# Kernel tuning notes

Measured on AMD Instinct MI355X. Metric: run time of the kernel, lower is better.

Reference implementation:

```python
import jax, jax.numpy as jnp
import numpy as np

EMB = 1024
HEADS = 16
HEAD_DIM = EMB // HEADS
SEQ = 2048
BATCH = 2
EPS = 1e-5


def gelu_tanh(x):
    # 0.5*x*(1+tanh(sqrt(2/pi)*(x+0.044715*x^3)))
    c = jnp.sqrt(jnp.asarray(2.0 / jnp.pi, x.dtype))
    return 0.5 * x * (1.0 + jnp.tanh(c * (x + 0.044715 * x * x * x)))


def layernorm(x, scale, shift):
    mean = jnp.mean(x, axis=-1, keepdims=True)
    # torch var(unbiased=True) -> ddof=1
    var = jnp.var(x, axis=-1, keepdims=True, ddof=1)
    return scale * (x - mean) / jnp.sqrt(var + EPS) + shift


def setup_inputs() -> dict:
    key = jax.random.key(0)
    ks = jax.random.split(key, 12)
    s = 0.02
    d = {
        "x": jax.random.normal(ks[0], (BATCH, SEQ, EMB), jnp.float32),
        "Wq": jax.random.normal(ks[1], (EMB, EMB), jnp.float32) * s,
        "bq": jnp.zeros((EMB,), jnp.float32),
        "Wk": jax.random.normal(ks[2], (EMB, EMB), jnp.float32) * s,
        "bk": jnp.zeros((EMB,), jnp.float32),
        "Wv": jax.random.normal(ks[3], (EMB, EMB), jnp.float32) * s,
        "bv": jnp.zeros((EMB,), jnp.float32),
        "Wo": jax.random.normal(ks[4], (EMB, EMB), jnp.float32) * s,
        "bo": jnp.zeros((EMB,), jnp.float32),
        "W1": jax.random.normal(ks[5], (EMB, 4 * EMB), jnp.float32) * s,
        "b1": jnp.zeros((4 * EMB,), jnp.float32),
        "W2": jax.random.normal(ks[6], (4 * EMB, EMB), jnp.float32) * s,
        "b2": jnp.zeros((EMB,), jnp.float32),
        "ln1_scale": jnp.ones((EMB,), jnp.float32),
        "ln1_shift": jnp.zeros((EMB,), jnp.float32),
        "ln2_scale": jnp.ones((EMB,), jnp.float32),
        "ln2_shift": jnp.zeros((EMB,), jnp.float32),
    }
    return d


def reference(x, Wq, bq, Wk, bk, Wv, bv, Wo, bo, W1, b1, W2, b2,
              ln1_scale, ln1_shift, ln2_scale, ln2_shift):
    b, n, _ = x.shape

    # --- attention sub-block (pre-norm) ---
    h = layernorm(x, ln1_scale, ln1_shift)
    q = (h @ Wq + bq).reshape(b, n, HEADS, HEAD_DIM).transpose(0, 2, 1, 3)
    k = (h @ Wk + bk).reshape(b, n, HEADS, HEAD_DIM).transpose(0, 2, 1, 3)
    v = (h @ Wv + bv).reshape(b, n, HEADS, HEAD_DIM).transpose(0, 2, 1, 3)

    # explicit O(n^2) scores, as in the source
    scores = jnp.einsum("bhqd,bhkd->bhqk", q, k)
    causal = jnp.triu(jnp.ones((n, n), bool), k=1)  # True above diagonal -> masked
    scores = jnp.where(causal, -jnp.inf, scores)
    weights = jax.nn.softmax(scores / jnp.sqrt(jnp.asarray(HEAD_DIM, x.dtype)), axis=-1)
    ctx = jnp.einsum("bhqk,bhkd->bhqd", weights, v)
    ctx = ctx.transpose(0, 2, 1, 3).reshape(b, n, EMB)
    x = x + (ctx @ Wo + bo)  # dropout is identity (rate 0 / eval)

    # --- FFN sub-block (pre-norm) ---
    h = layernorm(x, ln2_scale, ln2_shift)
    h = gelu_tanh(h @ W1 + b1)
    x = x + (h @ W2 + b2)
    return x
```

## Files before the change

kernel.cpp:

```cpp
#include <hip/hip_runtime.h>
#include <hip/hip_bf16.h>

#define EMB 1024
#define SEQ 2048
#define BATCH 2
#define HEADS 16
#define HDIM 64
#define ROWS (BATCH*SEQ)

typedef __hip_bfloat16 bf16;
typedef __bf16 bf16x8 __attribute__((ext_vector_type(8)));
typedef float f32x4 __attribute__((ext_vector_type(4)));

#define AS1 __attribute__((address_space(1)))
#define AS3 __attribute__((address_space(3)))

__device__ __forceinline__ void load_lds16(const void* g, void* l) {
    __builtin_amdgcn_global_load_lds((const AS1 void*)g, (AS3 void*)l, 16, 0, 0);
}

__device__ __forceinline__ float gelu_f(float x) {
    float y = 1.5957691216057308f * (x + 0.044715f * x * x * x);
    return x / (1.0f + __expf(-y));
}

__global__ void transpose_cast_kernel(const float* __restrict__ in, bf16* __restrict__ out,
                                      int R, int C) {
    __shared__ bf16 tile[32][33];
    int tx = threadIdx.x, ty = threadIdx.y;
    int c0 = blockIdx.x * 32, r0 = blockIdx.y * 32;
    for (int i = ty; i < 32; i += 8)
        tile[i][tx] = (bf16)in[(size_t)(r0 + i) * C + c0 + tx];
    __syncthreads();
    for (int i = ty; i < 32; i += 8)
        out[(size_t)(c0 + i) * R + r0 + tx] = tile[tx][i];
}

__global__ void transpose_cast4_kernel(const float* __restrict__ w0, const float* __restrict__ w1,
                                       const float* __restrict__ w2, const float* __restrict__ w3,
                                       bf16* __restrict__ o0, bf16* __restrict__ o1,
                                       bf16* __restrict__ o2, bf16* __restrict__ o3) {
    __shared__ bf16 tile[32][33];
    int z = blockIdx.z;
    const float* in = (z == 0) ? w0 : (z == 1) ? w1 : (z == 2) ? w2 : w3;
    bf16* out = (z == 0) ? o0 : (z == 1) ? o1 : (z == 2) ? o2 : o3;
    int tx = threadIdx.x, ty = threadIdx.y;
    int c0 = blockIdx.x * 32, r0 = blockIdx.y * 32;
    for (int i = ty; i < 32; i += 8)
        tile[i][tx] = (bf16)in[(size_t)(r0 + i) * 1024 + c0 + tx];
    __syncthreads();
    for (int i = ty; i < 32; i += 8)
        out[(size_t)(c0 + i) * 1024 + r0 + tx] = tile[tx][i];
}

__global__ void transpose_v_kernel(const bf16* __restrict__ v, bf16* __restrict__ vt) {
    __shared__ bf16 tile[32][33];
    int tx = threadIdx.x, ty = threadIdx.y;
    int bh = blockIdx.z;
    const bf16* in = v + (size_t)(bh >> 4) * SEQ * EMB + (bh & 15) * HDIM;
    bf16* out = vt + (size_t)bh * HDIM * SEQ;
    int s0 = blockIdx.x * 32, d0 = blockIdx.y * 32;
    for (int i = ty; i < 32; i += 8)
        tile[i][tx] = in[(size_t)(s0 + i) * EMB + d0 + tx];
    __syncthreads();
    for (int i = ty; i < 32; i += 8)
        out[(size_t)(d0 + i) * SEQ + s0 + tx] = tile[tx][i];
}

__global__ __launch_bounds__(256) void layernorm_kernel(const float* __restrict__ x,
                                                        bf16* __restrict__ out,
                                                        const float* __restrict__ scale,
                                                        const float* __restrict__ shift) {
    int row = blockIdx.x;
    int t = threadIdx.x;
    const float* xr = x + (size_t)row * EMB;
    float v[4];
    float s = 0.f, s2 = 0.f;
#pragma unroll
    for (int i = 0; i < 4; i++) {
        v[i] = xr[t + 256 * i];
        s += v[i];
        s2 += v[i] * v[i];
    }
#pragma unroll
    for (int off = 32; off > 0; off >>= 1) {
        s += __shfl_down(s, off);
        s2 += __shfl_down(s2, off);
    }
    __shared__ float sh[8];
    __shared__ float stats[2];
    int lane = t & 63, wid = t >> 6;
    if (lane == 0) { sh[wid] = s; sh[wid + 4] = s2; }
    __syncthreads();
    if (t == 0) {
        float ts = sh[0] + sh[1] + sh[2] + sh[3];
        float ts2 = sh[4] + sh[5] + sh[6] + sh[7];
        float mean = ts / (float)EMB;
        float var = (ts2 - (float)EMB * mean * mean) / (float)(EMB - 1);
        stats[0] = mean;
        stats[1] = rsqrtf(var + 1e-5f);
    }
    __syncthreads();
    float mean = stats[0], inv = stats[1];
#pragma unroll
    for (int i = 0; i < 4; i++) {
        int c = t + 256 * i;
        float y = (v[i] - mean) * inv * scale[c] + shift[c];
        out[(size_t)row * EMB + c] = (bf16)y;
    }
}

__device__ __forceinline__ void swz64(int id, int& bx, int& by) {
    int xcd = id & 7, m = id >> 3;
    by = xcd + 8 * (m & 3) + 32 * (m >> 6);
    bx = (m >> 2) & 15;
}

__device__ __forceinline__ void stage_half(const bf16* g, bf16* lds, int tid, size_t rowK64) {
    load_lds16(g, lds + tid * 8);
    load_lds16(g + rowK64, lds + 4096 + tid * 8);
}

template <int ACT, int QKV>
__global__ __launch_bounds__(512, 2) void gemm256_kernel(
    const bf16* __restrict__ A, const bf16* __restrict__ BT,
    bf16* __restrict__ C0, bf16* __restrict__ C1, bf16* __restrict__ C2,
    const float* __restrict__ bias0, const float* __restrict__ bias1,
    const float* __restrict__ bias2, int N, int K) {
    __shared__ __align__(16) bf16 lA[4][128 * 64];
    __shared__ __align__(16) bf16 lB[4][128 * 64];
    const int tid = threadIdx.x;
    const int wave = tid >> 6, lane = tid & 63;
    const int an = lane & 15, aq = lane >> 4;
    const int wr = wave >> 2, wc = wave & 3;

    int id = blockIdx.x;
    int xcd = id & 7, m = id >> 3;
    int by = xcd * 2 + (m & 1);
    int bx = m >> 1;
    int m0 = by * 256, n0 = bx * 256;

    const int srow = tid >> 3;
    const int csw = ((tid & 7) ^ (srow & 7)) * 8;
    const bf16* Ag = A + (size_t)(m0 + srow) * K + csw;
    const bf16* Bg = BT + (size_t)(n0 + srow) * K + csw;
    const size_t rowK64 = (size_t)64 * K;
    const size_t rowK128 = (size_t)128 * K;

    stage_half(Bg, lB[0], tid, rowK64);
    stage_half(Bg + rowK128, lB[1], tid, rowK64);
    stage_half(Ag, lA[0], tid, rowK64);
    stage_half(Ag + rowK128, lA[1], tid, rowK64);
    stage_half(Bg + 64, lB[2], tid, rowK64);
    stage_half(Bg + rowK128 + 64, lB[3], tid, rowK64);
    asm volatile("s_waitcnt vmcnt(4)" ::: "memory");
    __builtin_amdgcn_s_barrier();

    f32x4 acc[8][4] = {};
    const int NT = K >> 6;
    const int lrB = (wc & 1) * 64;

    for (int t = 0; t < NT; ++t) {
        const bf16* As = lA[(2 * t + wr) & 3];
        const bf16* Bs = lB[(2 * t + (wc >> 1)) & 3];
        bf16x8 bfv[4][2];
#pragma unroll
        for (int p = 0; p < 4; ++p) {
            bf16x8 af[2][2];
            if (p == 0) {
#pragma unroll
                for (int j = 0; j < 4; ++j)
#pragma unroll
                    for (int kk = 0; kk < 2; ++kk) {
                        int r = lrB + 16 * j + an;
                        bfv[j][kk] = *(const bf16x8*)(Bs + r * 64 + ((kk * 4 + aq) ^ (r & 7)) * 8);
                    }
            }
#pragma unroll
            for (int ii = 0; ii < 2; ++ii)
#pragma unroll
                for (int kk = 0; kk < 2; ++kk) {
                    int r = 16 * (2 * p + ii) + an;
                    af[ii][kk] = *(const bf16x8*)(As + r * 64 + ((kk * 4 + aq) ^ (r & 7)) * 8);
                }
            if (p == 0) {
                if (t + 1 < NT)
                    stage_half(Ag + (size_t)(t + 1) * 64, lA[(2 * t + 2) & 3], tid, rowK64);
            } else if (p == 1) {
                if (t + 1 < NT)
                    stage_half(Ag + rowK128 + (size_t)(t + 1) * 64, lA[(2 * t + 3) & 3], tid, rowK64);
            } else if (p == 2) {
                if (t + 2 < NT)
                    stage_half(Bg + (size_t)(t + 2) * 64, lB[(2 * t + 4) & 3], tid, rowK64);
            } else {
                if (t + 2 < NT) {
                    stage_half(Bg + rowK128 + (size_t)(t + 2) * 64, lB[(2 * t + 5) & 3], tid, rowK64);
                    asm volatile("s_waitcnt vmcnt(4)" ::: "memory");
                } else {
                    asm volatile("s_waitcnt vmcnt(0)" ::: "memory");
                }
            }
            __builtin_amdgcn_s_barrier();
            asm volatile("s_waitcnt lgkmcnt(0)" ::: "memory");
            __builtin_amdgcn_s_setprio(1);
#pragma unroll
            for (int ii = 0; ii < 2; ++ii)
#pragma unroll
                for (int j = 0; j < 4; ++j)
#pragma unroll
                    for (int kk = 0; kk < 2; ++kk)
                        acc[2 * p + ii][j] = __builtin_amdgcn_mfma_f32_16x16x32_bf16(
                            af[ii][kk], bfv[j][kk], acc[2 * p + ii][j], 0, 0, 0);
            __builtin_amdgcn_s_setprio(0);
            __builtin_amdgcn_s_barrier();
        }
    }

#pragma unroll
    for (int j = 0; j < 4; ++j) {
        int col = n0 + wc * 64 + 16 * j + an;
        if (QKV == 0) {
            float bv = bias0[col];
#pragma unroll
            for (int i = 0; i < 8; ++i) {
#pragma unroll
                for (int r = 0; r < 4; ++r) {
                    int row = m0 + wr * 128 + 16 * i + aq * 4 + r;
                    float v = acc[i][j][r] + bv;
                    if (ACT == 1) v = gelu_f(v);
                    C0[(size_t)row * N + col] = (bf16)v;
                }
            }
        } else {
            int region = col >> 10, c = col & 1023;
            const float* bp = (region == 0) ? bias0 : (region == 1) ? bias1 : bias2;
            bf16* outp = (region == 0) ? C0 : (region == 1) ? C1 : C2;
            float scl = (region == 0) ? 0.125f : 1.0f;
            float bv = bp[c];
#pragma unroll
            for (int i = 0; i < 8; ++i) {
#pragma unroll
                for (int r = 0; r < 4; ++r) {
                    int row = m0 + wr * 128 + 16 * i + aq * 4 + r;
                    float v = (acc[i][j][r] + bv) * scl;
                    outp[(size_t)row * EMB + c] = (bf16)v;
                }
            }
        }
    }
}

template <int RES, int OUTF>
__global__ __launch_bounds__(256) void gemm64_kernel(const bf16* __restrict__ A,
                                                     const bf16* __restrict__ BT,
                                                     void* __restrict__ Cout,
                                                     const float* __restrict__ bias,
                                                     const float* __restrict__ res,
                                                     int M, int N, int K) {
    __shared__ __align__(16) bf16 lA[2][2][64 * 32];
    __shared__ __align__(16) bf16 lB[2][2][64 * 32];
    int tid = threadIdx.x;
    int wave = tid >> 6, lane = tid & 63;
    int bx, by;
    swz64(blockIdx.x, bx, by);
    int m0 = by * 64, n0 = bx * 64;
    int wm = (wave >> 1) * 32, wn = (wave & 1) * 32;
    f32x4 acc[2][2] = {};

    int srow = wave * 16 + (lane >> 2);
    int skc = (lane & 3) * 8;
    const bf16* Ag = A + (size_t)(m0 + srow) * K + skc;
    const bf16* Bg = BT + (size_t)(n0 + srow) * K + skc;
    size_t woff = (size_t)(wave * 16) * 32;

    const int an = lane & 15;
    const int ak = (lane >> 4) * 8;

    load_lds16(Ag, &lA[0][0][woff]);
    load_lds16(Ag + 32, &lA[0][1][woff]);
    load_lds16(Bg, &lB[0][0][woff]);
    load_lds16(Bg + 32, &lB[0][1][woff]);

    int nsteps = K >> 6;
    for (int t = 0; t < nsteps; t++) {
        int buf = t & 1;
        asm volatile("s_waitcnt vmcnt(0)" ::: "memory");
        __syncthreads();
        if (t + 1 < nsteps) {
            int k0 = (t + 1) * 64;
            load_lds16(Ag + k0, &lA[buf ^ 1][0][woff]);
            load_lds16(Ag + k0 + 32, &lA[buf ^ 1][1][woff]);
            load_lds16(Bg + k0, &lB[buf ^ 1][0][woff]);
            load_lds16(Bg + k0 + 32, &lB[buf ^ 1][1][woff]);
        }
#pragma unroll
        for (int h = 0; h < 2; h++) {
            bf16x8 af[2], bfv[2];
#pragma unroll
            for (int i = 0; i < 2; i++)
                af[i] = *(const bf16x8*)(&lA[buf][h][(wm + 16 * i + an) * 32 + ak]);
#pragma unroll
            for (int j = 0; j < 2; j++)
                bfv[j] = *(const bf16x8*)(&lB[buf][h][(wn + 16 * j + an) * 32 + ak]);
#pragma unroll
            for (int i = 0; i < 2; i++)
#pragma unroll
                for (int j = 0; j < 2; j++)
                    acc[i][j] = __builtin_amdgcn_mfma_f32_16x16x32_bf16(af[i], bfv[j], acc[i][j], 0, 0, 0);
        }
    }
#pragma unroll
    for (int j = 0; j < 2; j++) {
        int col = n0 + wn + 16 * j + an;
        float bv = bias[col];
#pragma unroll
        for (int i = 0; i < 2; i++) {
#pragma unroll
            for (int r = 0; r < 4; r++) {
                int row = m0 + wm + 16 * i + (lane >> 4) * 4 + r;
                float vx = acc[i][j][r] + bv;
                size_t idx = (size_t)row * N + col;
                if (RES == 2) vx += res[idx];
                if (OUTF == 0) ((bf16*)Cout)[idx] = (bf16)vx;
                else ((float*)Cout)[idx] = vx;
            }
        }
    }
}

__global__ __launch_bounds__(256, 4) void attn_kernel(const bf16* __restrict__ q,
                                                      const bf16* __restrict__ k,
                                                      const bf16* __restrict__ vt,
                                                      bf16* __restrict__ ctx) {
    __shared__ __align__(16) bf16 ksm[2][64 * 64];
    __shared__ __align__(16) bf16 vsm[2][64 * 64];
    __shared__ __align__(16) bf16 pbuf[4][16][40];
    int tid = threadIdx.x;
    int wave = tid >> 6, lane = tid & 63;
    int id = blockIdx.x;
    int bh = id >> 5;
    int bx = ((id & 31) + bh) & 31;
    int b = bh >> 4, h = bh & 15;
    int q0 = bx * 64 + wave * 16;
    const bf16* qp = q + (size_t)b * SEQ * EMB + h * HDIM;
    const bf16* kp = k + (size_t)b * SEQ * EMB + h * HDIM;
    const bf16* vp = vt + (size_t)bh * HDIM * SEQ;

    int an = lane & 15, aq = lane >> 4;

    bf16x8 qf0 = *(const bf16x8*)(qp + (size_t)(q0 + an) * EMB + aq * 8);
    bf16x8 qf1 = *(const bf16x8*)(qp + (size_t)(q0 + an) * EMB + 32 + aq * 8);
    f32x4 o[4] = {};
    float lp[4] = {0.f, 0.f, 0.f, 0.f};

    int srow0 = tid >> 3;
    int srow1 = srow0 + 32;
    int sc = tid & 7;
    const bf16* kg0 = kp + (size_t)srow0 * EMB + ((sc ^ (srow0 & 7)) * 8);
    const bf16* kg1 = kp + (size_t)srow1 * EMB + ((sc ^ (srow1 & 7)) * 8);
    const bf16* vg0 = vp + (size_t)srow0 * SEQ + ((sc ^ (srow0 & 7)) * 8);
    const bf16* vg1 = vp + (size_t)srow1 * SEQ + ((sc ^ (srow1 & 7)) * 8);

    int nsteps = bx + 1;

    load_lds16(kg0, ksm[0] + tid * 8);
    load_lds16(kg1, ksm[0] + (256 + tid) * 8);
    load_lds16(vg0, vsm[0] + tid * 8);
    load_lds16(vg1, vsm[0] + (256 + tid) * 8);
    asm volatile("s_waitcnt vmcnt(0)" ::: "memory");
    __syncthreads();

    auto step = [&](int t, bool last_) {
        int buf = t & 1;
        if (!last_) {
            size_t ko = (size_t)(t + 1) * 64 * EMB;
            int vo = (t + 1) * 64;
            load_lds16(kg0 + ko, ksm[buf ^ 1] + tid * 8);
            load_lds16(kg1 + ko, ksm[buf ^ 1] + (256 + tid) * 8);
            load_lds16(vg0 + vo, vsm[buf ^ 1] + tid * 8);
            load_lds16(vg1 + vo, vsm[buf ^ 1] + (256 + tid) * 8);
        }
        const bf16* kb = ksm[buf];
        const bf16* vb = vsm[buf];
        int kvbase = t * 64;
#pragma unroll
        for (int hh = 0; hh < 2; hh++) {
#pragma unroll
            for (int nbl = 0; nbl < 2; nbl++) {
                int nb = hh * 2 + nbl;
                int krow = nb * 16 + an;
                bf16x8 kfa = *(const bf16x8*)(kb + krow * 64 + ((aq ^ (an & 7)) * 8));
                bf16x8 kfb = *(const bf16x8*)(kb + krow * 64 + (((4 + aq) ^ (an & 7)) * 8));
                f32x4 s = {};
                s = __builtin_amdgcn_mfma_f32_16x16x32_bf16(qf0, kfa, s, 0, 0, 0);
                s = __builtin_amdgcn_mfma_f32_16x16x32_bf16(qf1, kfb, s, 0, 0, 0);
                int kvg = kvbase + nb * 16 + an;
#pragma unroll
                for (int r = 0; r < 4; r++) {
                    float p = __expf(s[r]);
                    if (last_ && (kvg > q0 + aq * 4 + r)) p = 0.f;
                    lp[r] += p;
                    pbuf[wave][aq * 4 + r][nbl * 16 + an] = (bf16)p;
                }
            }
            asm volatile("s_waitcnt lgkmcnt(0)" ::: "memory");
            bf16x8 pa = *(const bf16x8*)(&pbuf[wave][an][aq * 8]);
#pragma unroll
            for (int dt = 0; dt < 4; dt++) {
                int drow = dt * 16 + an;
                bf16x8 vf = *(const bf16x8*)(vb + drow * 64 + (((hh * 4 + aq) ^ (an & 7)) * 8));
                o[dt] = __builtin_amdgcn_mfma_f32_16x16x32_bf16(pa, vf, o[dt], 0, 0, 0);
            }
        }
        if (!last_) {
            asm volatile("s_waitcnt vmcnt(0)" ::: "memory");
            __syncthreads();
        }
    };

    for (int t = 0; t < nsteps - 1; t++) step(t, false);
    step(nsteps - 1, true);

#pragma unroll
    for (int r = 0; r < 4; r++) {
        float v = lp[r];
        v += __shfl_xor(v, 1);
        v += __shfl_xor(v, 2);
        v += __shfl_xor(v, 4);
        v += __shfl_xor(v, 8);
        lp[r] = v;
    }
#pragma unroll
    for (int dt = 0; dt < 4; dt++) {
#pragma unroll
        for (int r = 0; r < 4; r++) {
            int row = q0 + aq * 4 + r;
            int col = h * HDIM + dt * 16 + an;
            ctx[((size_t)b * SEQ + row) * EMB + col] = (bf16)(o[dt][r] / lp[r]);
        }
    }
}

extern "C" void kernel_launch(void* const* d_in, const int* in_sizes, int n_in,
                              void* d_out, int out_size, void* d_ws, size_t ws_size,
                              hipStream_t stream) {
    const float* x = (const float*)d_in[0];
    const float* Wq = (const float*)d_in[1];
    const float* bq = (const float*)d_in[2];
    const float* Wk = (const float*)d_in[3];
    const float* bk = (const float*)d_in[4];
    const float* Wv = (const float*)d_in[5];
    const float* bv = (const float*)d_in[6];
    const float* Wo = (const float*)d_in[7];
    const float* bo = (const float*)d_in[8];
    const float* W1 = (const float*)d_in[9];
    const float* b1 = (const float*)d_in[10];
    const float* W2 = (const float*)d_in[11];
    const float* b2 = (const float*)d_in[12];
    const float* ln1s = (const float*)d_in[13];
    const float* ln1b = (const float*)d_in[14];
    const float* ln2s = (const float*)d_in[15];
    const float* ln2b = (const float*)d_in[16];
    float* out = (float*)d_out;

    char* ws = (char*)d_ws;
    const size_t MB = 1ull << 20;
    bf16* WqT = (bf16*)(ws + 0 * MB);
    bf16* WkT = (bf16*)(ws + 2 * MB);
    bf16* WvT = (bf16*)(ws + 4 * MB);
    bf16* WoT = (bf16*)(ws + 6 * MB);
    bf16* W1T = (bf16*)(ws + 8 * MB);
    bf16* W2T = (bf16*)(ws + 16 * MB);
    bf16* hbuf = (bf16*)(ws + 24 * MB);
    bf16* qbuf = (bf16*)(ws + 32 * MB);
    bf16* kbuf = (bf16*)(ws + 40 * MB);
    bf16* vbuf = (bf16*)(ws + 48 * MB);
    bf16* vtb = (bf16*)(ws + 56 * MB);
    bf16* ctxb = (bf16*)(ws + 64 * MB);
    float* x1 = (float*)(ws + 72 * MB);
    bf16* hff = (bf16*)(ws + 32 * MB);

    dim3 tb(32, 8);
    transpose_cast4_kernel<<<dim3(32, 32, 4), tb, 0, stream>>>(Wq, Wk, Wv, Wo, WqT, WkT, WvT, WoT);
    transpose_cast_kernel<<<dim3(128, 32), tb, 0, stream>>>(W1, W1T, 1024, 4096);
    transpose_cast_kernel<<<dim3(32, 128), tb, 0, stream>>>(W2, W2T, 4096, 1024);

    layernorm_kernel<<<ROWS, 256, 0, stream>>>(x, hbuf, ln1s, ln1b);

    gemm256_kernel<0, 1><<<192, 512, 0, stream>>>(hbuf, WqT, qbuf, kbuf, vbuf,
                                                  bq, bk, bv, EMB, EMB);

    transpose_v_kernel<<<dim3(64, 2, 32), tb, 0, stream>>>(vbuf, vtb);

    attn_kernel<<<1024, 256, 0, stream>>>(qbuf, kbuf, vtb, ctxb);

    gemm64_kernel<2, 1><<<1024, 256, 0, stream>>>(ctxb, WoT, x1, bo, x, ROWS, EMB, EMB);

    layernorm_kernel<<<ROWS, 256, 0, stream>>>(x1, hbuf, ln2s, ln2b);

    gemm256_kernel<1, 0><<<256, 512, 0, stream>>>(hbuf, W1T, hff, nullptr, nullptr,
                                                  b1, nullptr, nullptr, 4 * EMB, EMB);

    gemm64_kernel<2, 1><<<1024, 256, 0, stream>>>(hff, W2T, out, b2, x1, ROWS, EMB, 4 * EMB);
}
```

Measured before the change: 354.4 us.

## Process two query sub-tiles per attention block to reuse K/V tiles

Each attention block now handles 128 query rows (two 64-row groups, each wave covering two 16-row slices) instead of 64, so every K/V tile loaded into LDS feeds twice as many MFMAs. The grid halves to 512 blocks. The last two KV steps use special modes so the diagonal tiles are masked correctly and the fully-masked tile is skipped for the first group. The cost is more registers (launch bounds drop to 2 blocks per CU), fewer blocks and coarser causal load imbalance.

```diff
diff --git a/kernel.cpp b/kernel.cpp
--- a/kernel.cpp
+++ b/kernel.cpp
@@ -328,30 +328,34 @@
     }
 }
 
-__global__ __launch_bounds__(256, 4) void attn_kernel(const bf16* __restrict__ q,
+__global__ __launch_bounds__(256, 2) void attn_kernel(const bf16* __restrict__ q,
                                                       const bf16* __restrict__ k,
                                                       const bf16* __restrict__ vt,
                                                       bf16* __restrict__ ctx) {
     __shared__ __align__(16) bf16 ksm[2][64 * 64];
     __shared__ __align__(16) bf16 vsm[2][64 * 64];
-    __shared__ __align__(16) bf16 pbuf[4][16][40];
+    __shared__ __align__(16) bf16 pbuf[2][4][16][40];
     int tid = threadIdx.x;
     int wave = tid >> 6, lane = tid & 63;
     int id = blockIdx.x;
-    int bh = id >> 5;
-    int bx = ((id & 31) + bh) & 31;
+    int bh = id >> 4;
+    int bx = ((id & 15) + bh) & 15;
     int b = bh >> 4, h = bh & 15;
-    int q0 = bx * 64 + wave * 16;
+    int q0 = bx * 128 + wave * 16;
     const bf16* qp = q + (size_t)b * SEQ * EMB + h * HDIM;
     const bf16* kp = k + (size_t)b * SEQ * EMB + h * HDIM;
     const bf16* vp = vt + (size_t)bh * HDIM * SEQ;
 
     int an = lane & 15, aq = lane >> 4;
 
-    bf16x8 qf0 = *(const bf16x8*)(qp + (size_t)(q0 + an) * EMB + aq * 8);
-    bf16x8 qf1 = *(const bf16x8*)(qp + (size_t)(q0 + an) * EMB + 32 + aq * 8);
-    f32x4 o[4] = {};
-    float lp[4] = {0.f, 0.f, 0.f, 0.f};
+    bf16x8 qf[2][2];
+#pragma unroll
+    for (int g = 0; g < 2; g++) {
+        qf[g][0] = *(const bf16x8*)(qp + (size_t)(q0 + 64 * g + an) * EMB + aq * 8);
+        qf[g][1] = *(const bf16x8*)(qp + (size_t)(q0 + 64 * g + an) * EMB + 32 + aq * 8);
+    }
+    f32x4 o[2][4] = {};
+    float lp[2][4] = {};
 
     int srow0 = tid >> 3;
     int srow1 = srow0 + 32;
@@ -361,7 +365,7 @@
     const bf16* vg0 = vp + (size_t)srow0 * SEQ + ((sc ^ (srow0 & 7)) * 8);
     const bf16* vg1 = vp + (size_t)srow1 * SEQ + ((sc ^ (srow1 & 7)) * 8);
 
-    int nsteps = bx + 1;
+    int nsteps = 2 * bx + 2;
 
     load_lds16(kg0, ksm[0] + tid * 8);
     load_lds16(kg1, ksm[0] + (256 + tid) * 8);
@@ -370,9 +374,9 @@
     asm volatile("s_waitcnt vmcnt(0)" ::: "memory");
     __syncthreads();
 
-    auto step = [&](int t, bool last_) {
+    auto step = [&](int t, int mode) {
         int buf = t & 1;
-        if (!last_) {
+        if (t + 1 < nsteps) {
             size_t ko = (size_t)(t + 1) * 64 * EMB;
             int vo = (t + 1) * 64;
             load_lds16(kg0 + ko, ksm[buf ^ 1] + tid * 8);
@@ -386,59 +390,72 @@
 #pragma unroll
         for (int hh = 0; hh < 2; hh++) {
 #pragma unroll
-            for (int nbl = 0; nbl < 2; nbl++) {
-                int nb = hh * 2 + nbl;
-                int krow = nb * 16 + an;
-                bf16x8 kfa = *(const bf16x8*)(kb + krow * 64 + ((aq ^ (an & 7)) * 8));
-                bf16x8 kfb = *(const bf16x8*)(kb + krow * 64 + (((4 + aq) ^ (an & 7)) * 8));
-                f32x4 s = {};
-                s = __builtin_amdgcn_mfma_f32_16x16x32_bf16(qf0, kfa, s, 0, 0, 0);
-                s = __builtin_amdgcn_mfma_f32_16x16x32_bf16(qf1, kfb, s, 0, 0, 0);
-                int kvg = kvbase + nb * 16 + an;
-#pragma unroll
-                for (int r = 0; r < 4; r++) {
-                    float p = __expf(s[r]);
-                    if (last_ && (kvg > q0 + aq * 4 + r)) p = 0.f;
-                    lp[r] += p;
-                    pbuf[wave][aq * 4 + r][nbl * 16 + an] = (bf16)p;
+            for (int g = 0; g < 2; g++) {
+                if (mode == 2 && g == 0) continue;
+                bool msk = (mode == 1 && g == 0) || (mode == 2 && g == 1);
+#pragma unroll
+                for (int nbl = 0; nbl < 2; nbl++) {
+                    int nb = hh * 2 + nbl;
+                    int krow = nb * 16 + an;
+                    bf16x8 kfa = *(const bf16x8*)(kb + krow * 64 + ((aq ^ (an & 7)) * 8));
+                    bf16x8 kfb = *(const bf16x8*)(kb + krow * 64 + (((4 + aq) ^ (an & 7)) * 8));
+                    f32x4 s = {};
+                    s = __builtin_amdgcn_mfma_f32_16x16x32_bf16(qf[g][0], kfa, s, 0, 0, 0);
+                    s = __builtin_amdgcn_mfma_f32_16x16x32_bf16(qf[g][1], kfb, s, 0, 0, 0);
+                    int kvg = kvbase + nb * 16 + an;
+#pragma unroll
+                    for (int r = 0; r < 4; r++) {
+                        float p = __expf(s[r]);
+                        if (msk && (kvg > q0 + 64 * g + aq * 4 + r)) p = 0.f;
+                        lp[g][r] += p;
+                        pbuf[g][wave][aq * 4 + r][nbl * 16 + an] = (bf16)p;
+                    }
                 }
             }
             asm volatile("s_waitcnt lgkmcnt(0)" ::: "memory");
-            bf16x8 pa = *(const bf16x8*)(&pbuf[wave][an][aq * 8]);
+            bf16x8 pa0 = *(const bf16x8*)(&pbuf[0][wave][an][aq * 8]);
+            bf16x8 pa1 = *(const bf16x8*)(&pbuf[1][wave][an][aq * 8]);
 #pragma unroll
             for (int dt = 0; dt < 4; dt++) {
                 int drow = dt * 16 + an;
                 bf16x8 vf = *(const bf16x8*)(vb + drow * 64 + (((hh * 4 + aq) ^ (an & 7)) * 8));
-                o[dt] = __builtin_amdgcn_mfma_f32_16x16x32_bf16(pa, vf, o[dt], 0, 0, 0);
-            }
-        }
-        if (!last_) {
+                if (mode != 2)
+                    o[0][dt] = __builtin_amdgcn_mfma_f32_16x16x32_bf16(pa0, vf, o[0][dt], 0, 0, 0);
+                o[1][dt] = __builtin_amdgcn_mfma_f32_16x16x32_bf16(pa1, vf, o[1][dt], 0, 0, 0);
+            }
+        }
+        if (t + 1 < nsteps) {
             asm volatile("s_waitcnt vmcnt(0)" ::: "memory");
             __syncthreads();
         }
     };
 
-    for (int t = 0; t < nsteps - 1; t++) step(t, false);
-    step(nsteps - 1, true);
-
-#pragma unroll
-    for (int r = 0; r < 4; r++) {
-        float v = lp[r];
-        v += __shfl_xor(v, 1);
-        v += __shfl_xor(v, 2);
-        v += __shfl_xor(v, 4);
-        v += __shfl_xor(v, 8);
-        lp[r] = v;
-    }
-#pragma unroll
-    for (int dt = 0; dt < 4; dt++) {
+    for (int t = 0; t < nsteps - 2; t++) step(t, 0);
+    step(nsteps - 2, 1);
+    step(nsteps - 1, 2);
+
+#pragma unroll
+    for (int g = 0; g < 2; g++)
 #pragma unroll
         for (int r = 0; r < 4; r++) {
-            int row = q0 + aq * 4 + r;
-            int col = h * HDIM + dt * 16 + an;
-            ctx[((size_t)b * SEQ + row) * EMB + col] = (bf16)(o[dt][r] / lp[r]);
-        }
-    }
+            float v = lp[g][r];
+            v += __shfl_xor(v, 1);
+            v += __shfl_xor(v, 2);
+            v += __shfl_xor(v, 4);
+            v += __shfl_xor(v, 8);
+            lp[g][r] = v;
+        }
+#pragma unroll
+    for (int g = 0; g < 2; g++)
+#pragma unroll
+        for (int dt = 0; dt < 4; dt++) {
+#pragma unroll
+            for (int r = 0; r < 4; r++) {
+                int row = q0 + 64 * g + aq * 4 + r;
+                int col = h * HDIM + dt * 16 + an;
+                ctx[((size_t)b * SEQ + row) * EMB + col] = (bf16)(o[g][dt][r] / lp[g][r]);
+            }
+        }
 }
 
 extern "C" void kernel_launch(void* const* d_in, const int* in_sizes, int n_in,
@@ -492,7 +509,7 @@
 
     transpose_v_kernel<<<dim3(64, 2, 32), tb, 0, stream>>>(vbuf, vtb);
 
-    attn_kernel<<<1024, 256, 0, stream>>>(qbuf, kbuf, vtb, ctxb);
+    attn_kernel<<<512, 256, 0, stream>>>(qbuf, kbuf, vtb, ctxb);
 
     gemm64_kernel<2, 1><<<1024, 256, 0, stream>>>(ctxb, WoT, x1, bo, x, ROWS, EMB, EMB);
 
```

Result: no change. 361.0 us (+1.8%).
